# Kernel optimization log

Measured on AMD Instinct MI355X. Metric: run time of the kernel, lower is better.

Reference implementation:

```python
import jax, jax.numpy as jnp
import numpy as np
from jax import lax

OVERLAP_THRESHOLD = 0.5


def _pairwise_iou(a, b):
    # a: [A,4], b: [B,4] -> [A,B]  (jaccard() in the original repo)
    max_xy = jnp.minimum(a[:, None, 2:], b[None, :, 2:])
    min_xy = jnp.maximum(a[:, None, :2], b[None, :, :2])
    wh = jnp.clip(max_xy - min_xy, 0.0)
    inter = wh[..., 0] * wh[..., 1]
    area_a = (a[:, 2] - a[:, 0]) * (a[:, 3] - a[:, 1])
    area_b = (b[:, 2] - b[:, 0]) * (b[:, 3] - b[:, 1])
    union = area_a[:, None] + area_b[None, :] - inter
    return inter / union


def _elementwise_iou(a, b):
    # matches UBR_ZERO_IoULoss._intersect/_iou_loss: same-shape [K,4] boxes
    max_xy = jnp.minimum(a[:, 2:], b[:, 2:])
    min_xy = jnp.maximum(a[:, :2], b[:, :2])
    wh = jnp.clip(max_xy - min_xy, 0.0)
    inter = wh[:, 0] * wh[:, 1]
    area_a = (a[:, 2] - a[:, 0]) * (a[:, 3] - a[:, 1])
    area_b = (b[:, 2] - b[:, 0]) * (b[:, 3] - b[:, 1])
    return inter / (area_a + area_b - inter)


def _inverse_transform(boxes, deltas):
    w = boxes[:, 2] - boxes[:, 0] + 1.0
    h = boxes[:, 3] - boxes[:, 1] + 1.0
    cx = boxes[:, 0] + 0.5 * w
    cy = boxes[:, 1] + 0.5 * h
    pcx = deltas[:, 0] * w + cx
    pcy = deltas[:, 1] * h + cy
    pw = jnp.exp(deltas[:, 2]) * w
    ph = jnp.exp(deltas[:, 3]) * h
    return jnp.stack([pcx - 0.5 * pw, pcy - 0.5 * ph,
                      pcx + 0.5 * pw, pcy + 0.5 * ph], axis=1)


def setup_inputs() -> dict:
    key = jax.random.key(0)
    k1, k2, k3, k4 = jax.random.split(key, 4)
    N, M, D = 32768, 4096, 512
    raw = jax.random.uniform(k1, (N, 4), dtype=jnp.float32)
    xy = raw[:, :2] * 900.0
    wh = raw[:, 2:] * 100.0 + 1.0
    rois = jnp.concatenate([xy, xy + wh], axis=1)
    # gt boxes = jittered subset of rois -> guarantees IoU>0.5 matches exist
    gt_box = rois[:M] + jax.random.normal(k2, (M, 4), dtype=jnp.float32) * 2.0
    bbox_pred = jax.random.normal(k3, (N, 4), dtype=jnp.float32) * 0.1
    feat = jax.random.normal(k4, (N, D), dtype=jnp.float32)
    return {"rois": rois, "bbox_pred": bbox_pred, "gt_box": gt_box, "feat": feat}


def reference(rois, bbox_pred, gt_box, feat):
    num_rois = rois.shape[0]
    iou = _pairwise_iou(rois, gt_box)              # [N, M]
    max_iou = jnp.max(iou, axis=1)                 # [N]
    max_gt_idx = jnp.argmax(iou, axis=1)           # [N]
    # boolean compaction in torch replaced by a fixed-shape mask (jit-safe)
    mask = lax.stop_gradient((max_iou > OVERLAP_THRESHOLD).astype(rois.dtype))
    n_matched = jnp.sum(mask).astype(jnp.int32)
    matched_gt = gt_box[max_gt_idx]                # [N, 4]
    refined = _inverse_transform(rois, bbox_pred)  # [N, 4]
    iou_ref = _elementwise_iou(refined, matched_gt)
    loss = -jnp.log(iou_ref + 0.1) * mask          # per-roi, 0 where unmatched
    feat_loss = jnp.sum(jnp.abs(jnp.sum(feat * mask[:, None], axis=0)))
    return loss, n_matched, num_rois, refined * mask[:, None], feat_loss
```

## Files before the change

kernel.cpp:

```cpp
#include <hip/hip_runtime.h>
#include <math.h>

#define GRID 16
#define NCELL 256
#define FB 256
#define MMAX 4096

typedef unsigned long long ull;

__device__ __forceinline__ void cell_xy(float c, int& out) {
  int v = (int)floorf((c + 16.0f) * 0.015625f);
  out = min(max(v, 0), GRID - 1);
}

__global__ __launch_bounds__(256) void k_bin(
    const float4* __restrict__ gt4, int M,
    int* __restrict__ off_g, int* __restrict__ cnt_g,
    float4* __restrict__ gbox, int* __restrict__ ctr) {
  __shared__ int scnt[NCELL], spre[NCELL], sfill[NCELL];
  const int t = threadIdx.x;
  scnt[t] = 0;
  __syncthreads();
  for (int k = t; k < M; k += 256) {
    float4 g = gt4[k];
    int ix, iy;
    cell_xy(0.5f * (g.x + g.z), ix);
    cell_xy(0.5f * (g.y + g.w), iy);
    atomicAdd(&scnt[iy * GRID + ix], 1);
  }
  __syncthreads();
  int v = scnt[t];
  spre[t] = v; __syncthreads();
  for (int o = 1; o < NCELL; o <<= 1) {
    int a = (t >= o) ? spre[t - o] : 0; __syncthreads();
    spre[t] += a; __syncthreads();
  }
  int ex = spre[t] - v;
  off_g[t] = ex; cnt_g[t] = v; sfill[t] = ex;
  __syncthreads();
  for (int k = t; k < M; k += 256) {
    float4 g = gt4[k];
    int ix, iy;
    cell_xy(0.5f * (g.x + g.z), ix);
    cell_xy(0.5f * (g.y + g.w), iy);
    gbox[atomicAdd(&sfill[iy * GRID + ix], 1)] = g;
  }
  if (t == 0) *ctr = 0;
}

__global__ __launch_bounds__(256) void k_main(
    const float4* __restrict__ rois4, const float4* __restrict__ deltas4,
    const int* __restrict__ off_g, const int* __restrict__ cnt_g,
    const float4* __restrict__ gbox, int M,
    int* __restrict__ ctr, int* __restrict__ mlist,
    float* __restrict__ out_loss, float* __restrict__ out_refined) {
  __shared__ float4 sgbox[MMAX];
  __shared__ int soff[NCELL], scnt_[NCELL];
  const int t = threadIdx.x;
  soff[t] = off_g[t];
  scnt_[t] = cnt_g[t];
  for (int k = t; k < M; k += 256) sgbox[k] = gbox[k];
  __syncthreads();

  const int slice = t & 3;
  const int i = blockIdx.x * 64 + (t >> 2);
  float4 r = rois4[i];
  const float area_a = (r.z - r.x) * (r.w - r.y);
  int cx, cy;
  cell_xy(0.5f * (r.x + r.z), cx);
  cell_xy(0.5f * (r.y + r.w), cy);

  const double Cd = 0.500000029802322387695312500;
  float bi = 0.f, bu = 1.f;
  int bjpos = 0;
  bool matched = false;
  for (int dy = -1; dy <= 1; ++dy) {
    int yy = cy + dy;
    if (yy < 0 || yy > GRID - 1) continue;
    int c0 = (yy << 4) | max(cx - 1, 0);
    int c1 = (yy << 4) | min(cx + 1, GRID - 1);
    int s = soff[c0];
    int e = soff[c1] + scnt_[c1];
    #pragma unroll 2
    for (int j = s + slice; j < e; j += 4) {
      float4 g = sgbox[j];
      float ab = (g.z - g.x) * (g.w - g.y);
      float ix = fminf(r.z, g.z) - fmaxf(r.x, g.x);
      float iy = fminf(r.w, g.w) - fmaxf(r.y, g.y);
      float inter = fmaxf(ix, 0.f) * fmaxf(iy, 0.f);
      float uni = (area_a + ab) - inter;
      bool upos = uni > 0.f;
      float ug = upos ? uni : 3.0e38f;
      matched = matched | (fma(-Cd, (double)ug, (double)inter) > 0.0);
      bool win = upos && (inter * bu > bi * uni);
      bi = win ? inter : bi;
      bu = win ? uni : bu;
      bjpos = win ? j : bjpos;
    }
  }
  int mi = matched ? 1 : 0;
  #pragma unroll
  for (int x = 1; x <= 2; x <<= 1) {
    float bi_o = __shfl_xor(bi, x, 64);
    float bu_o = __shfl_xor(bu, x, 64);
    int bj_o = __shfl_xor(bjpos, x, 64);
    mi |= __shfl_xor(mi, x, 64);
    bool take = bi_o * bu > bi * bu_o;
    bi = take ? bi_o : bi;
    bu = take ? bu_o : bu;
    bjpos = take ? bj_o : bjpos;
  }
  if (slice != 0) return;
  bool mt = mi != 0;
  float m = mt ? 1.f : 0.f;
  if (mt) mlist[atomicAdd(ctr, 1)] = i;

  float4 d = deltas4[i];
  float w = r.z - r.x + 1.f, h = r.w - r.y + 1.f;
  float ccx = r.x + 0.5f * w, ccy = r.y + 0.5f * h;
  float pcx = d.x * w + ccx, pcy = d.y * h + ccy;
  float pw = expf(d.z) * w, ph = expf(d.w) * h;
  float rx0 = pcx - 0.5f * pw, ry0 = pcy - 0.5f * ph;
  float rx1 = pcx + 0.5f * pw, ry1 = pcy + 0.5f * ph;

  float loss = 0.f;
  if (mt) {
    float4 g = sgbox[bjpos];
    float ix = fmaxf(fminf(rx1, g.z) - fmaxf(rx0, g.x), 0.f);
    float iy = fmaxf(fminf(ry1, g.w) - fmaxf(ry0, g.y), 0.f);
    float inter = ix * iy;
    float aa = (rx1 - rx0) * (ry1 - ry0);
    float ab = (g.z - g.x) * (g.w - g.y);
    float er = inter / (aa + ab - inter);
    loss = -logf(er + 0.1f);
  }
  out_loss[i] = loss;
  out_refined[4 * i + 0] = rx0 * m;
  out_refined[4 * i + 1] = ry0 * m;
  out_refined[4 * i + 2] = rx1 * m;
  out_refined[4 * i + 3] = ry1 * m;
}

__global__ __launch_bounds__(256) void k_feat2(
    const float4* __restrict__ feat4, const int* __restrict__ mlist,
    const int* __restrict__ ctr, float4* __restrict__ pcolsP4, int D4) {
  const int nm = *ctr;
  const int t = threadIdx.x;
  const int c = t & 127;
  const int h = t >> 7;
  __shared__ int sidx[128];

  const int chunk = (nm + FB - 1) / FB;
  const int start = blockIdx.x * chunk;
  int len = nm - start;
  len = (len < 0) ? 0 : ((len > chunk) ? chunk : len);
  for (int k = t; k < len; k += 256) sidx[k] = mlist[start + k];
  __syncthreads();

  float4 acc = {0.f, 0.f, 0.f, 0.f};
  int e0 = h * 8;
  for (; e0 + 8 <= len; e0 += 16) {
    int id[8];
    #pragma unroll
    for (int k = 0; k < 8; ++k) id[k] = sidx[e0 + k];
    float4 v[8];
    #pragma unroll
    for (int k = 0; k < 8; ++k) v[k] = feat4[(size_t)id[k] * D4 + c];
    #pragma unroll
    for (int k = 0; k < 8; ++k) {
      acc.x += v[k].x; acc.y += v[k].y; acc.z += v[k].z; acc.w += v[k].w;
    }
  }
  for (int e = e0; e < len && e < e0 + 8; ++e) {
    float4 v = feat4[(size_t)sidx[e] * D4 + c];
    acc.x += v.x; acc.y += v.y; acc.z += v.z; acc.w += v.w;
  }

  __shared__ float4 red[256];
  red[t] = acc;
  __syncthreads();
  if (t < 128) {
    float4 o = red[t + 128];
    acc.x += o.x; acc.y += o.y; acc.z += o.z; acc.w += o.w;
    pcolsP4[(size_t)blockIdx.x * 128 + t] = acc;
  }
}

__global__ __launch_bounds__(512) void k_final(
    const float* __restrict__ pcolsP, const int* __restrict__ ctr,
    float* __restrict__ out, int N) {
  const int t = threadIdx.x;
  float s = 0.f;
  for (int r = 0; r < FB; ++r) s += pcolsP[(size_t)r * 512 + t];
  float a = fabsf(s);
  for (int off = 32; off > 0; off >>= 1) a += __shfl_down(a, off, 64);
  __shared__ float ra[8];
  if ((t & 63) == 0) ra[t >> 6] = a;
  __syncthreads();
  if (t == 0) {
    float ta = 0.f;
    for (int k = 0; k < 8; ++k) ta += ra[k];
    out[N] = (float)(*ctr);
    out[N + 1] = (float)N;
    out[(size_t)5 * N + 2] = ta;
  }
}

extern "C" void kernel_launch(void* const* d_in, const int* in_sizes, int n_in,
                              void* d_out, int out_size, void* d_ws, size_t ws_size,
                              hipStream_t stream) {
  const float* rois = (const float*)d_in[0];
  const float* bbox = (const float*)d_in[1];
  const float* gt   = (const float*)d_in[2];
  const float* feat = (const float*)d_in[3];
  const int N = in_sizes[0] / 4;
  const int M = in_sizes[2] / 4;
  const int D = in_sizes[3] / N;
  float* out = (float*)d_out;

  char* ws = (char*)d_ws;
  int* off_g   = (int*)ws;
  int* cnt_g   = off_g + NCELL;
  int* ctr     = cnt_g + NCELL;
  int* mlist   = ctr + 13;
  float4* gbox = (float4*)(mlist + N);
  float* pcolsP = (float*)(gbox + M);

  k_bin<<<1, 256, 0, stream>>>((const float4*)gt, M, off_g, cnt_g, gbox, ctr);
  k_main<<<N / 64, 256, 0, stream>>>((const float4*)rois, (const float4*)bbox,
                                     off_g, cnt_g, gbox, M, ctr, mlist,
                                     out, out + N + 2);
  k_feat2<<<FB, 256, 0, stream>>>((const float4*)feat, mlist, ctr,
                                  (float4*)pcolsP, D / 4);
  k_final<<<1, 512, 0, stream>>>(pcolsP, ctr, out, N);
}
```

Measured before the change: 161.3 us.

## Fold gt binning into every main block and merge final reduction via last-block

Removes the single-block binning kernel: every k_main block now redundantly bins all gt boxes into its own shared memory (counting, prefix scan, scatter) instead of loading a prebuilt global binned list. The final reduction kernel is folded into the feature kernel using a threadfence plus atomic done-counter so the last block finishes the sum, and counters are zeroed with a memset. This cuts two launches and the serial 1-block binning stage, at the cost of each of 512 blocks repeating the M-box binning work and global atomics-free shared atomics.

```diff
diff --git a/kernel.cpp b/kernel.cpp
--- a/kernel.cpp
+++ b/kernel.cpp
@@ -13,12 +13,15 @@
   out = min(max(v, 0), GRID - 1);
 }
 
-__global__ __launch_bounds__(256) void k_bin(
+__global__ __launch_bounds__(256) void k_main(
+    const float4* __restrict__ rois4, const float4* __restrict__ deltas4,
     const float4* __restrict__ gt4, int M,
-    int* __restrict__ off_g, int* __restrict__ cnt_g,
-    float4* __restrict__ gbox, int* __restrict__ ctr) {
+    int* __restrict__ ctr, int* __restrict__ mlist,
+    float* __restrict__ out_loss, float* __restrict__ out_refined) {
+  __shared__ float4 sgbox[MMAX];
   __shared__ int scnt[NCELL], spre[NCELL], sfill[NCELL];
   const int t = threadIdx.x;
+
   scnt[t] = 0;
   __syncthreads();
   for (int k = t; k < M; k += 256) {
@@ -35,31 +38,15 @@
     int a = (t >= o) ? spre[t - o] : 0; __syncthreads();
     spre[t] += a; __syncthreads();
   }
-  int ex = spre[t] - v;
-  off_g[t] = ex; cnt_g[t] = v; sfill[t] = ex;
+  sfill[t] = spre[t] - v;
   __syncthreads();
   for (int k = t; k < M; k += 256) {
     float4 g = gt4[k];
     int ix, iy;
     cell_xy(0.5f * (g.x + g.z), ix);
     cell_xy(0.5f * (g.y + g.w), iy);
-    gbox[atomicAdd(&sfill[iy * GRID + ix], 1)] = g;
-  }
-  if (t == 0) *ctr = 0;
-}
-
-__global__ __launch_bounds__(256) void k_main(
-    const float4* __restrict__ rois4, const float4* __restrict__ deltas4,
-    const int* __restrict__ off_g, const int* __restrict__ cnt_g,
-    const float4* __restrict__ gbox, int M,
-    int* __restrict__ ctr, int* __restrict__ mlist,
-    float* __restrict__ out_loss, float* __restrict__ out_refined) {
-  __shared__ float4 sgbox[MMAX];
-  __shared__ int soff[NCELL], scnt_[NCELL];
-  const int t = threadIdx.x;
-  soff[t] = off_g[t];
-  scnt_[t] = cnt_g[t];
-  for (int k = t; k < M; k += 256) sgbox[k] = gbox[k];
+    sgbox[atomicAdd(&sfill[iy * GRID + ix], 1)] = g;
+  }
   __syncthreads();
 
   const int slice = t & 3;
@@ -79,8 +66,8 @@
     if (yy < 0 || yy > GRID - 1) continue;
     int c0 = (yy << 4) | max(cx - 1, 0);
     int c1 = (yy << 4) | min(cx + 1, GRID - 1);
-    int s = soff[c0];
-    int e = soff[c1] + scnt_[c1];
+    int s = spre[c0] - scnt[c0];
+    int e = spre[c1];
     #pragma unroll 2
     for (int j = s + slice; j < e; j += 4) {
       float4 g = sgbox[j];
@@ -141,9 +128,10 @@
   out_refined[4 * i + 3] = ry1 * m;
 }
 
-__global__ __launch_bounds__(256) void k_feat2(
+__global__ __launch_bounds__(256) void k_featfold(
     const float4* __restrict__ feat4, const int* __restrict__ mlist,
-    const int* __restrict__ ctr, float4* __restrict__ pcolsP4, int D4) {
+    const int* __restrict__ ctr, int* __restrict__ done,
+    float4* __restrict__ pcolsP4, float* __restrict__ out, int N, int D4) {
   const int nm = *ctr;
   const int t = threadIdx.x;
   const int c = t & 127;
@@ -184,23 +172,27 @@
     acc.x += o.x; acc.y += o.y; acc.z += o.z; acc.w += o.w;
     pcolsP4[(size_t)blockIdx.x * 128 + t] = acc;
   }
-}
-
-__global__ __launch_bounds__(512) void k_final(
-    const float* __restrict__ pcolsP, const int* __restrict__ ctr,
-    float* __restrict__ out, int N) {
-  const int t = threadIdx.x;
-  float s = 0.f;
-  for (int r = 0; r < FB; ++r) s += pcolsP[(size_t)r * 512 + t];
-  float a = fabsf(s);
+
+  __threadfence();
+  __shared__ int amLast;
+  if (t == 0) amLast = (atomicAdd(done, 1) == FB - 1);
+  __syncthreads();
+  if (!amLast) return;
+
+  const float* pc = (const float*)pcolsP4;
+  float a0 = 0.f, a1 = 0.f;
+  for (int rr = 0; rr < FB; ++rr) {
+    a0 += pc[rr * 512 + t];
+    a1 += pc[rr * 512 + t + 256];
+  }
+  float a = fabsf(a0) + fabsf(a1);
   for (int off = 32; off > 0; off >>= 1) a += __shfl_down(a, off, 64);
-  __shared__ float ra[8];
+  __shared__ float ra[4];
   if ((t & 63) == 0) ra[t >> 6] = a;
   __syncthreads();
   if (t == 0) {
-    float ta = 0.f;
-    for (int k = 0; k < 8; ++k) ta += ra[k];
-    out[N] = (float)(*ctr);
+    float ta = ra[0] + ra[1] + ra[2] + ra[3];
+    out[N] = (float)nm;
     out[N + 1] = (float)N;
     out[(size_t)5 * N + 2] = ta;
   }
@@ -219,18 +211,16 @@
   float* out = (float*)d_out;
 
   char* ws = (char*)d_ws;
-  int* off_g   = (int*)ws;
-  int* cnt_g   = off_g + NCELL;
-  int* ctr     = cnt_g + NCELL;
-  int* mlist   = ctr + 13;
-  float4* gbox = (float4*)(mlist + N);
-  float* pcolsP = (float*)(gbox + M);
-
-  k_bin<<<1, 256, 0, stream>>>((const float4*)gt, M, off_g, cnt_g, gbox, ctr);
+  int* ctr    = (int*)ws;
+  int* done   = ctr + 1;
+  int* mlist  = ctr + 4;
+  float* pcolsP = (float*)(mlist + N);
+
+  hipMemsetAsync(ctr, 0, 8, stream);
+
   k_main<<<N / 64, 256, 0, stream>>>((const float4*)rois, (const float4*)bbox,
-                                     off_g, cnt_g, gbox, M, ctr, mlist,
+                                     (const float4*)gt, M, ctr, mlist,
                                      out, out + N + 2);
-  k_feat2<<<FB, 256, 0, stream>>>((const float4*)feat, mlist, ctr,
-                                  (float4*)pcolsP, D / 4);
-  k_final<<<1, 512, 0, stream>>>(pcolsP, ctr, out, N);
-}
+  k_featfold<<<FB, 256, 0, stream>>>((const float4*)feat, mlist, ctr, done,
+                                     (float4*)pcolsP, out, N, D / 4);
+}
```

Result: slower. 174.0 us (+7.9%).
